# Kernel tuning notes

Hardware: AMD Instinct MI355X
Metric: run time of the kernel (lower is better)

Reference implementation:

```python
import jax, jax.numpy as jnp
import numpy as np

BT, N = 4, 2048
FIN, FOUT = 512, 128          # GGE in/out; FOUT == PPI output (GAGA constraint)
PIN, POUT = 256, 128          # PPIGE in/out
HEAD = 4
K = POUT // HEAD              # per-head dim = 32
NEG_SLOPE = 0.2
MASK_VAL = -1e30


def setup_inputs() -> dict:
    key = jax.random.key(0)
    ks = jax.random.split(key, 24)
    s = 0.05
    inp = {}
    inp["a"] = jax.random.normal(ks[0], (BT, FIN), jnp.float32)
    inp["bio_a"] = jax.random.normal(ks[1], (BT, N, PIN), jnp.float32)
    inp["A"] = jax.random.randint(ks[2], (BT, N, N), 0, 2, jnp.int32)
    inp["b"] = jax.random.normal(ks[3], (BT, FIN), jnp.float32)
    inp["bio_b"] = jax.random.normal(ks[4], (BT, N, PIN), jnp.float32)
    inp["B"] = jax.random.randint(ks[5], (BT, N, N), 0, 2, jnp.int32)
    # PPIGE_GAT params (shared across both graph branches)
    inp["initW"] = jax.random.normal(ks[6], (POUT, PIN), jnp.float32) * s
    inp["initb"] = jnp.zeros((POUT,), jnp.float32)
    inp["projW"] = jax.random.normal(ks[7], (POUT, POUT), jnp.float32) * s  # no bias
    inp["attw"] = jax.random.normal(ks[8], (HEAD, 2 * K), jnp.float32) * s  # per-head [2k]->1
    inp["attb"] = jnp.zeros((HEAD,), jnp.float32)
    # GGE params
    inp["ggeW1"] = jax.random.normal(ks[9], (128, FIN), jnp.float32) * s
    inp["ggeb1"] = jnp.zeros((128,), jnp.float32)
    inp["ggeW2"] = jax.random.normal(ks[10], (FOUT, 128), jnp.float32) * s
    inp["ggeb2"] = jnp.zeros((FOUT,), jnp.float32)
    # LED params (hidden = FOUT)
    inp["convW"] = jax.random.normal(ks[11], (2 * FOUT, 2 * FOUT), jnp.float32) * s  # k=1 conv
    inp["convb"] = jnp.zeros((2 * FOUT,), jnp.float32)
    inp["ledW1"] = jax.random.normal(ks[12], (FOUT, 4 * FOUT), jnp.float32) * s
    inp["ledb1"] = jnp.zeros((FOUT,), jnp.float32)
    inp["ledW2"] = jax.random.normal(ks[13], (2, FOUT), jnp.float32) * s
    inp["ledb2"] = jnp.zeros((2,), jnp.float32)
    return inp


def _gat_layer(x, adj_mask, projW, attw, attb):
    # x: [B,N,POUT]; adj_mask: [B,N,N] bool
    Bt, n, _ = x.shape
    xh = (x @ projW.T).reshape(Bt, n, HEAD, K).transpose(0, 2, 1, 3)  # [B,h,N,k]
    # score(i,j) = leaky_relu(w1.x_i + w2.x_j + b)  (equivalent to Linear on concat)
    s1 = jnp.einsum('bhnk,hk->bhn', xh, attw[:, :K])
    s2 = jnp.einsum('bhnk,hk->bhn', xh, attw[:, K:])
    scores = jax.nn.leaky_relu(
        s1[..., :, None] + s2[..., None, :] + attb[None, :, None, None], NEG_SLOPE)
    scores = jnp.where(adj_mask[:, None], scores, MASK_VAL)
    att = jax.nn.softmax(scores, axis=-1)                     # [B,h,N,N]
    out = jax.nn.relu(att @ xh)                               # [B,h,N,k]
    return out.transpose(0, 2, 1, 3).reshape(Bt, n, HEAD * K)


def _ppige(bio, adj, initW, initb, projW, attw, attb):
    x = bio @ initW.T + initb
    return _gat_layer(x, adj > 0, projW, attw, attb) + x      # residual; dropout=eval


def _gge(a, W1, b1, W2, b2):
    h = jax.nn.relu(a @ W1.T + b1)
    return jax.nn.relu(h @ W2.T + b2)


def _gaga(G, h):
    # G: [B,N,D], h: [B,D]
    att = jax.nn.softmax(jnp.einsum('bnd,bd->bn', G, h), axis=-1)
    return jnp.einsum('bnd,bn->bd', G, att)


def _led(ea, eb, convW, convb, W1, b1, W2, b2):
    # pointwise conv over the length-2 stack [ea, eb], then maxpool over length
    cnn = jnp.maximum(ea @ convW.T + convb, eb @ convW.T + convb)  # [B,2D]
    x = jax.nn.relu(jnp.concatenate([cnn, ea - eb], axis=1) @ W1.T + b1)
    return x @ W2.T + b2


def reference(a, bio_a, A, b, bio_b, B,
              initW, initb, projW, attw, attb,
              ggeW1, ggeb1, ggeW2, ggeb2,
              convW, convb, ledW1, ledb1, ledW2, ledb2):
    G_a = _ppige(bio_a, A, initW, initb, projW, attw, attb)
    G_b = _ppige(bio_b, B, initW, initb, projW, attw, attb)
    h_a = _gge(a, ggeW1, ggeb1, ggeW2, ggeb2)
    h_b = _gge(b, ggeW1, ggeb1, ggeW2, ggeb2)
    e_a = jnp.concatenate([h_a, _gaga(G_a, h_a)], axis=-1)
    e_b = jnp.concatenate([h_b, _gaga(G_b, h_b)], axis=-1)
    logits = _led(e_a, e_b, convW, convb, ledW1, ledb1, ledW2, ledb2)
    return jax.nn.log_softmax(logits, axis=-1)
```

## Files before the change

kernel.cpp:

```cpp
#include <hip/hip_runtime.h>
#include <hip/hip_bf16.h>
#include <math.h>

#define NN 2048
#define NEG 0.2f
#define LOG2E 1.44269504f

typedef short bf16x8 __attribute__((ext_vector_type(8)));
typedef float f32x16 __attribute__((ext_vector_type(16)));

__device__ __forceinline__ float dot4(float4 a, float4 b) {
  return a.x * b.x + a.y * b.y + a.z * b.z + a.w * b.w;
}

__device__ __forceinline__ unsigned short bfbits(float f) {
  union { __hip_bfloat16 b; unsigned short u; } c;
  c.b = __float2bfloat16(f);
  return c.u;
}

__global__ __launch_bounds__(256) void k12_fused(const float* __restrict__ bioA,
                                                 const float* __restrict__ bioB,
                                                 const float* __restrict__ initW,
                                                 const float* __restrict__ initb,
                                                 const float* __restrict__ projW,
                                                 const float* __restrict__ attw,
                                                 const float* __restrict__ a_in,
                                                 const float* __restrict__ b_in,
                                                 const float* __restrict__ ggeW1,
                                                 const float* __restrict__ ggeb1,
                                                 const float* __restrict__ ggeW2,
                                                 const float* __restrict__ ggeb2,
                                                 float* __restrict__ xout,
                                                 unsigned short* __restrict__ xhT2,
                                                 float* __restrict__ s1,
                                                 float* __restrict__ s2,
                                                 float* __restrict__ hvbuf,
                                                 float* __restrict__ e) {
  __shared__ float As[32][36];
  __shared__ float Ws[32][132];
  __shared__ float xT[128][36];
  const int t = threadIdx.x;
  const int wave = t >> 6, lane = t & 63;

  if (blockIdx.x >= 512) {
    float* inL = (float*)As;
    float* h1L = ((float*)As) + 512;
    const int bb2 = (int)blockIdx.x - 512;
    const int g = bb2 >> 2, b = bb2 & 3;
    const int gb2 = g * 4 + b;
    const float* inp = (g ? b_in : a_in) + b * 512;
    if (t < 128) *(float4*)&inL[t * 4] = *(const float4*)&inp[t * 4];
    __syncthreads();
    for (int p = 0; p < 16; ++p) {
      const int o0 = p * 8 + wave * 2;
      const float* w0 = &ggeW1[o0 * 512 + lane * 8];
      const float* w1 = &ggeW1[(o0 + 1) * 512 + lane * 8];
      const float4 i0v = *(const float4*)&inL[lane * 8];
      const float4 i1v = *(const float4*)&inL[lane * 8 + 4];
      float s0 = dot4(*(const float4*)&w0[0], i0v) + dot4(*(const float4*)&w0[4], i1v);
      float s1v = dot4(*(const float4*)&w1[0], i0v) + dot4(*(const float4*)&w1[4], i1v);
#pragma unroll
      for (int s = 1; s < 64; s <<= 1) { s0 += __shfl_xor(s0, s); s1v += __shfl_xor(s1v, s); }
      if (lane == 0) {
        h1L[o0] = fmaxf(s0 + ggeb1[o0], 0.f);
        h1L[o0 + 1] = fmaxf(s1v + ggeb1[o0 + 1], 0.f);
      }
    }
    __syncthreads();
    for (int p = 0; p < 16; ++p) {
      const int o0 = p * 8 + wave * 2;
      const float2 w0 = *(const float2*)&ggeW2[o0 * 128 + lane * 2];
      const float2 w1 = *(const float2*)&ggeW2[(o0 + 1) * 128 + lane * 2];
      const float2 hvv = *(const float2*)&h1L[lane * 2];
      float s0 = w0.x * hvv.x + w0.y * hvv.y;
      float s1v = w1.x * hvv.x + w1.y * hvv.y;
#pragma unroll
      for (int s = 1; s < 64; s <<= 1) { s0 += __shfl_xor(s0, s); s1v += __shfl_xor(s1v, s); }
      if (lane == 0) {
        const float v0 = fmaxf(s0 + ggeb2[o0], 0.f);
        const float v1 = fmaxf(s1v + ggeb2[o0 + 1], 0.f);
        hvbuf[gb2 * 128 + o0] = v0;
        hvbuf[gb2 * 128 + o0 + 1] = v1;
        e[gb2 * 256 + o0] = v0;
        e[gb2 * 256 + o0 + 1] = v1;
      }
    }
    return;
  }

  const int m0 = blockIdx.x * 32;
  const float* A = (m0 < 8192) ? bioA : bioB;
  const int arow0 = (m0 < 8192) ? m0 : (m0 - 8192);
  const int og = t & 31, ig = t >> 5;

  float acc[4][4] = {};
  for (int kt = 0; kt < 256; kt += 32) {
    __syncthreads();
    {
      const int r = t >> 3, kq = t & 7;
      const float4 v = *(const float4*)&A[(arow0 + r) * 256 + kt + kq * 4];
      As[kq * 4 + 0][r] = v.x; As[kq * 4 + 1][r] = v.y;
      As[kq * 4 + 2][r] = v.z; As[kq * 4 + 3][r] = v.w;
    }
#pragma unroll
    for (int u = 0; u < 4; ++u) {
      const int f = u * 256 + t;
      const int o = f >> 3, kq = f & 7;
      const float4 v = *(const float4*)&initW[o * 256 + kt + kq * 4];
      Ws[kq * 4 + 0][o] = v.x; Ws[kq * 4 + 1][o] = v.y;
      Ws[kq * 4 + 2][o] = v.z; Ws[kq * 4 + 3][o] = v.w;
    }
    __syncthreads();
#pragma unroll
    for (int kk = 0; kk < 32; ++kk) {
      const float4 a4 = *(const float4*)&As[kk][ig * 4];
      const float4 w4 = *(const float4*)&Ws[kk][og * 4];
      const float av[4] = {a4.x, a4.y, a4.z, a4.w};
      const float wv[4] = {w4.x, w4.y, w4.z, w4.w};
#pragma unroll
      for (int ii = 0; ii < 4; ++ii)
#pragma unroll
        for (int jj = 0; jj < 4; ++jj) acc[ii][jj] += av[ii] * wv[jj];
    }
  }
  {
    const float4 b4 = *(const float4*)&initb[og * 4];
    const float bj[4] = {b4.x, b4.y, b4.z, b4.w};
#pragma unroll
    for (int ii = 0; ii < 4; ++ii) {
      const int row = m0 + ig * 4 + ii;
      float4 o4;
      o4.x = acc[ii][0] + bj[0]; o4.y = acc[ii][1] + bj[1];
      o4.z = acc[ii][2] + bj[2]; o4.w = acc[ii][3] + bj[3];
      *(float4*)&xout[row * 128 + og * 4] = o4;
    }
#pragma unroll
    for (int jj = 0; jj < 4; ++jj) {
      float4 v;
      v.x = acc[0][jj] + bj[jj]; v.y = acc[1][jj] + bj[jj];
      v.z = acc[2][jj] + bj[jj]; v.w = acc[3][jj] + bj[jj];
      *(float4*)&xT[og * 4 + jj][ig * 4] = v;
    }
  }
  __syncthreads();

  float acc2[4][4] = {};
  for (int kt = 0; kt < 128; kt += 32) {
    __syncthreads();
#pragma unroll
    for (int u = 0; u < 4; ++u) {
      const int f = u * 256 + t;
      const int o = f >> 3, kq = f & 7;
      const float4 v = *(const float4*)&projW[o * 128 + kt + kq * 4];
      Ws[kq * 4 + 0][o] = v.x; Ws[kq * 4 + 1][o] = v.y;
      Ws[kq * 4 + 2][o] = v.z; Ws[kq * 4 + 3][o] = v.w;
    }
    __syncthreads();
#pragma unroll
    for (int kk = 0; kk < 32; ++kk) {
      const float4 a4 = *(const float4*)&xT[kt + kk][ig * 4];
      const float4 w4 = *(const float4*)&Ws[kk][og * 4];
      const float av[4] = {a4.x, a4.y, a4.z, a4.w};
      const float wv[4] = {w4.x, w4.y, w4.z, w4.w};
#pragma unroll
      for (int ii = 0; ii < 4; ++ii)
#pragma unroll
        for (int jj = 0; jj < 4; ++jj) acc2[ii][jj] += av[ii] * wv[jj];
    }
  }
  const int h = og >> 3;
  const int k4i = (og & 7) * 4;
  const int g = m0 >> 13;
  const int bb = (m0 >> 11) & 3;
  const int gb = g * 4 + bb;
  const int n0 = (m0 & 2047) + ig * 4;
  const float4 w1 = *(const float4*)&attw[h * 64 + k4i];
  const float4 w2 = *(const float4*)&attw[h * 64 + 32 + k4i];
  float p1[4], p2[4];
#pragma unroll
  for (int ii = 0; ii < 4; ++ii) {
    float4 v;
    v.x = acc2[ii][0]; v.y = acc2[ii][1]; v.z = acc2[ii][2]; v.w = acc2[ii][3];
    p1[ii] = dot4(v, w1);
    p2[ii] = dot4(v, w2);
  }
  {
    const int mtile = n0 >> 4, jslot = (n0 >> 3) & 1, j8 = n0 & 7;
    const int base2 = ((((gb * 4 + h) * 128 + mtile) * 2 + jslot) * 32) * 8 + j8;
#pragma unroll
    for (int jj = 0; jj < 4; ++jj) {
      const int kin = k4i + jj;
      ushort4 u;
      u.x = bfbits(acc2[0][jj]); u.y = bfbits(acc2[1][jj]);
      u.z = bfbits(acc2[2][jj]); u.w = bfbits(acc2[3][jj]);
      *(ushort4*)&xhT2[base2 + kin * 8] = u;
    }
  }
#pragma unroll
  for (int s = 1; s < 8; s <<= 1) {
#pragma unroll
    for (int ii = 0; ii < 4; ++ii) {
      p1[ii] += __shfl_xor(p1[ii], s);
      p2[ii] += __shfl_xor(p2[ii], s);
    }
  }
  if ((og & 7) == 0) {
#pragma unroll
    for (int ii = 0; ii < 4; ++ii) {
      s1[(gb * 4 + h) * NN + n0 + ii] = p1[ii];
      s2[(gb * 4 + h) * NN + n0 + ii] = p2[ii];
    }
  }
}

#define K3_PROLOGUE                                                           \
  {                                                                           \
    const float* s2g = s2w + gb * 4 * NN;                                     \
    _Pragma("unroll")                                                         \
    for (int u = 0; u < 4; ++u) {                                             \
      const int idx = u * 2048 + t * 4;                                       \
      float4 v = *(const float4*)&s2g[idx];                                   \
      v.x *= LOG2E; v.y *= LOG2E; v.z *= LOG2E; v.w *= LOG2E;                 \
      *(float4*)&s2L[idx] = v;                                                \
    }                                                                         \
  }                                                                           \
  _Pragma("unroll")                                                           \
  for (int r4 = 0; r4 < 4; ++r4) {                                            \
    const int r = wave * 4 + r4;                                              \
    const int* arow = adj + r * NN;                                           \
    int av[32];                                                               \
    _Pragma("unroll")                                                         \
    for (int w = 0; w < 32; ++w) av[w] = __builtin_nontemporal_load(&arow[w * 64 + lane]); \
    _Pragma("unroll")                                                         \
    for (int w = 0; w < 32; ++w) {                                            \
      const unsigned long long mm = __ballot(av[w] > 0);                      \
      if (lane < 2) adjL[r * 66 + 2 * w + lane] = (unsigned int)(mm >> (32 * lane)); \
    }                                                                         \
  }

#define K3_SCORE_BODY(MM)                                                     \
    const int j0 = jlo + 16 * (MM) + jslot * 8;                               \
    const unsigned int wbits = adjL[i * 66 + ((jlo + 16 * (MM)) >> 5)];       \
    const unsigned int bits8 = wbits >> ((((MM) & 1) * 16) + jslot * 8);      \
    const float4 s2a = *(const float4*)&s2L[h * 2048 + j0];                   \
    const float4 s2b = *(const float4*)&s2L[h * 2048 + j0 + 4];               \
    const float sv[8] = {s2a.x, s2a.y, s2a.z, s2a.w,                          \
                         s2b.x, s2b.y, s2b.z, s2b.w};                         \
    union { bf16x8 v; unsigned short u[8]; } af;                              \
    float dsum = 0.f;                                                         \
    _Pragma("unroll")                                                         \
    for (int e = 0; e < 8; ++e) {                                             \
      float s = sc1v + sv[e];                                                 \
      s = fmaxf(s, NEG * s);                                                  \
      float pe = __builtin_amdgcn_exp2f(s);                                   \
      pe = ((bits8 >> e) & 1u) ? pe : 0.f;                                    \
      af.u[e] = bfbits(pe);                                                   \
      dsum += pe;                                                             \
    }                                                                         \
    den += dsum;

__global__ __launch_bounds__(512) void k3_attn(const unsigned short* __restrict__ xhT2,
                                               const float* __restrict__ s1w,
                                               const float* __restrict__ s2w,
                                               const int* __restrict__ adjA,
                                               const int* __restrict__ adjB,
                                               const float* __restrict__ attb,
                                               const float* __restrict__ x,
                                               const float* __restrict__ hv,
                                               float* __restrict__ G,
                                               float* __restrict__ wsumC,
                                               float* __restrict__ mzC) {
  __shared__ __align__(16) unsigned char smem3[42240];
  unsigned int* adjL = (unsigned int*)smem3;
  float* s2L = (float*)(smem3 + 8448);
  float* denR = (float*)(smem3 + 41216);
  float* accR = (float*)smem3;
  float* lgW = (float*)(smem3 + 16640);
  float* pL = (float*)(smem3 + 17280);

  const int t = threadIdx.x;
  const int wave = t >> 6, lane = t & 63;
  const int p = (int)blockIdx.x;
  const int blk = (p & 7) * 64 + (p >> 3);
  const int g = blk >> 8, b = (blk >> 6) & 3;
  const int i0 = (blk & 63) * 32;
  const int gb = g * 4 + b;
  const int cidx = gb * 64 + (blk & 63);
  const int* adj = (g ? adjB : adjA) + (b * NN + i0) * NN;
  K3_PROLOGUE
  __syncthreads();

  const int h = wave & 3;
  const int jhalf = wave >> 2;
  const int jlo = jhalf * 1024;
  const int i = lane & 31;
  const int jslot = lane >> 5;
  const float sc1v = (s1w[(gb * 4 + h) * NN + i0 + i] + attb[h]) * LOG2E;
  const unsigned short* bbase = xhT2 + (gb * 4 + h) * 65536 + jhalf * 32768 + lane * 8;
  f32x16 acc = {0.f, 0.f, 0.f, 0.f, 0.f, 0.f, 0.f, 0.f,
                0.f, 0.f, 0.f, 0.f, 0.f, 0.f, 0.f, 0.f};
  float den = 0.f;

#define K3_CSTEP(RB, MM)                                                      \
  {                                                                           \
    K3_SCORE_BODY(MM)                                                         \
    acc = __builtin_amdgcn_mfma_f32_32x32x16_bf16(af.v, RB, acc, 0, 0, 0);    \
  }

  bf16x8 fa0 = *(const bf16x8*)&bbase[0 * 512];
  bf16x8 fa1 = *(const bf16x8*)&bbase[1 * 512];
  bf16x8 fa2 = *(const bf16x8*)&bbase[2 * 512];
  bf16x8 fa3 = *(const bf16x8*)&bbase[3 * 512];
  bf16x8 fb0 = *(const bf16x8*)&bbase[4 * 512];
  bf16x8 fb1 = *(const bf16x8*)&bbase[5 * 512];
  bf16x8 fb2 = *(const bf16x8*)&bbase[6 * 512];
  bf16x8 fb3 = *(const bf16x8*)&bbase[7 * 512];
  bf16x8 fc0 = *(const bf16x8*)&bbase[8 * 512];
  bf16x8 fc1 = *(const bf16x8*)&bbase[9 * 512];
  bf16x8 fc2 = *(const bf16x8*)&bbase[10 * 512];
  bf16x8 fc3 = *(const bf16x8*)&bbase[11 * 512];
  bf16x8 fd0 = *(const bf16x8*)&bbase[12 * 512];
  bf16x8 fd1 = *(const bf16x8*)&bbase[13 * 512];
  bf16x8 fd2 = *(const bf16x8*)&bbase[14 * 512];
  bf16x8 fd3 = *(const bf16x8*)&bbase[15 * 512];
  __builtin_amdgcn_sched_barrier(0);
  for (int mb = 0; mb < 64; mb += 16) {
    K3_CSTEP(fa0, mb + 0)
    K3_CSTEP(fa1, mb + 1)
    K3_CSTEP(fa2, mb + 2)
    K3_CSTEP(fa3, mb + 3)
    __builtin_amdgcn_sched_barrier(0);
    if (mb < 48) {
      fa0 = *(const bf16x8*)&bbase[(mb + 16) * 512];
      fa1 = *(const bf16x8*)&bbase[(mb + 17) * 512];
      fa2 = *(const bf16x8*)&bbase[(mb + 18) * 512];
      fa3 = *(const bf16x8*)&bbase[(mb + 19) * 512];
    }
    __builtin_amdgcn_sched_barrier(0);
    K3_CSTEP(fb0, mb + 4)
    K3_CSTEP(fb1, mb + 5)
    K3_CSTEP(fb2, mb + 6)
    K3_CSTEP(fb3, mb + 7)
    __builtin_amdgcn_sched_barrier(0);
    if (mb < 48) {
      fb0 = *(const bf16x8*)&bbase[(mb + 20) * 512];
      fb1 = *(const bf16x8*)&bbase[(mb + 21) * 512];
      fb2 = *(const bf16x8*)&bbase[(mb + 22) * 512];
      fb3 = *(const bf16x8*)&bbase[(mb + 23) * 512];
    }
    __builtin_amdgcn_sched_barrier(0);
    K3_CSTEP(fc0, mb + 8)
    K3_CSTEP(fc1, mb + 9)
    K3_CSTEP(fc2, mb + 10)
    K3_CSTEP(fc3, mb + 11)
    __builtin_amdgcn_sched_barrier(0);
    if (mb < 48) {
      fc0 = *(const bf16x8*)&bbase[(mb + 24) * 512];
      fc1 = *(const bf16x8*)&bbase[(mb + 25) * 512];
      fc2 = *(const bf16x8*)&bbase[(mb + 26) * 512];
      fc3 = *(const bf16x8*)&bbase[(mb + 27) * 512];
    }
    __builtin_amdgcn_sched_barrier(0);
    K3_CSTEP(fd0, mb + 12)
    K3_CSTEP(fd1, mb + 13)
    K3_CSTEP(fd2, mb + 14)
    K3_CSTEP(fd3, mb + 15)
    __builtin_amdgcn_sched_barrier(0);
    if (mb < 48) {
      fd0 = *(const bf16x8*)&bbase[(mb + 28) * 512];
      fd1 = *(const bf16x8*)&bbase[(mb + 29) * 512];
      fd2 = *(const bf16x8*)&bbase[(mb + 30) * 512];
      fd3 = *(const bf16x8*)&bbase[(mb + 31) * 512];
    }
    __builtin_amdgcn_sched_barrier(0);
  }
#undef K3_CSTEP

  den += __shfl_xor(den, 32);
  if (lane < 32) denR[(h * 2 + jhalf) * 32 + lane] = den;
  __syncthreads();
  if (jhalf == 1) {
#pragma unroll
    for (int r = 0; r < 16; ++r) accR[(h * 16 + r) * 65 + lane] = acc[r];
  }
  __syncthreads();
  const float hvv = hv[gb * 128 + h * 32 + i];
  if (jhalf == 0) {
#pragma unroll
    for (int r = 0; r < 16; ++r) {
      const int row = (r & 3) + 8 * (r >> 2) + 4 * jslot;
      const float dinv = 1.f / (denR[(h * 2 + 0) * 32 + row] + denR[(h * 2 + 1) * 32 + row]);
      const int off = (gb * NN + i0 + row) * 128 + h * 32 + i;
      const float av2 = acc[r] + accR[(h * 16 + r) * 65 + lane];
      const float gval = fmaxf(av2 * dinv, 0.f) + x[off];
      G[off] = gval;
      float c = gval * hvv;
      c += __shfl_xor(c, 1); c += __shfl_xor(c, 2); c += __shfl_xor(c, 4);
      c += __shfl_xor(c, 8); c += __shfl_xor(c, 16);
      if (i == 0) lgW[h * 32 + row] = c;
    }
  }
  __syncthreads();
  if (t < 32) {
    float lg = lgW[t] + lgW[32 + t] + lgW[64 + t] + lgW[96 + t];
    float m = lg;
    m = fmaxf(m, __shfl_xor(m, 1)); m = fmaxf(m, __shfl_xor(m, 2));
    m = fmaxf(m, __shfl_xor(m, 4)); m = fmaxf(m, __shfl_xor(m, 8));
    m = fmaxf(m, __shfl_xor(m, 16));
    const float pv = __expf(lg - m);
    float z = pv;
    z += __shfl_xor(z, 1); z += __shfl_xor(z, 2); z += __shfl_xor(z, 4);
    z += __shfl_xor(z, 8); z += __shfl_xor(z, 16);
    pL[t] = pv;
    if (t == 0) { mzC[cidx * 2] = m; mzC[cidx * 2 + 1] = z; }
  }
  __syncthreads();
  if (jhalf == 0) {
    float wp = 0.f;
#pragma unroll
    for (int r = 0; r < 16; ++r) {
      const int row = (r & 3) + 8 * (r >> 2) + 4 * jslot;
      const int off = (gb * NN + i0 + row) * 128 + h * 32 + i;
      wp += pL[row] * G[off];
    }
    wp += __shfl_xor(wp, 32);
    if (jslot == 0) wsumC[cidx * 128 + h * 32 + i] = wp;
  }
}

__global__ __launch_bounds__(256) void k5_led(const float* __restrict__ e,
                                              const float* __restrict__ wsumC,
                                              const float* __restrict__ mzC,
                                              const float* __restrict__ convW,
                                              const float* __restrict__ convb,
                                              const float* __restrict__ ledW1,
                                              const float* __restrict__ ledb1,
                                              const float* __restrict__ ledW2,
                                              const float* __restrict__ ledb2,
                                              float* __restrict__ out) {
  __shared__ float eaL[256], ebL[256], uL[512], xL[128], lgL[2];
  const int t = threadIdx.x;
  const int wave = t >> 6, lane = t & 63;
  const int bt = blockIdx.x;
  const int gba = bt, gbb = 4 + bt;
  if (t < 128) {
    eaL[t] = e[gba * 256 + t];
    ebL[t] = e[gbb * 256 + t];
    float ma = -1e30f, mb2 = -1e30f;
    for (int c = 0; c < 64; ++c) {
      ma = fmaxf(ma, mzC[(gba * 64 + c) * 2]);
      mb2 = fmaxf(mb2, mzC[(gbb * 64 + c) * 2]);
    }
    float Za = 0.f, Zb = 0.f, sa = 0.f, sb = 0.f;
    for (int c = 0; c < 64; ++c) {
      const float wa = __expf(mzC[(gba * 64 + c) * 2] - ma);
      const float wb = __expf(mzC[(gbb * 64 + c) * 2] - mb2);
      Za += mzC[(gba * 64 + c) * 2 + 1] * wa;
      Zb += mzC[(gbb * 64 + c) * 2 + 1] * wb;
      sa += wsumC[(gba * 64 + c) * 128 + t] * wa;
      sb += wsumC[(gbb * 64 + c) * 128 + t] * wb;
    }
    eaL[128 + t] = sa / Za;
    ebL[128 + t] = sb / Zb;
  }
  __syncthreads();
  uL[256 + t] = eaL[t] - ebL[t];
  const float4 ea4 = *(const float4*)&eaL[lane * 4];
  const float4 eb4 = *(const float4*)&ebL[lane * 4];
  for (int p = 0; p < 32; ++p) {
    const int o0 = p * 8 + wave * 2;
    const float4 w0 = *(const float4*)&convW[o0 * 256 + lane * 4];
    const float4 w1 = *(const float4*)&convW[(o0 + 1) * 256 + lane * 4];
    float sa0 = dot4(w0, ea4), sb0 = dot4(w0, eb4);
    float sa1 = dot4(w1, ea4), sb1 = dot4(w1, eb4);
#pragma unroll
    for (int s = 1; s < 64; s <<= 1) {
      sa0 += __shfl_xor(sa0, s); sb0 += __shfl_xor(sb0, s);
      sa1 += __shfl_xor(sa1, s); sb1 += __shfl_xor(sb1, s);
    }
    if (lane == 0) {
      const float c0 = convb[o0], c1 = convb[o0 + 1];
      uL[o0] = fmaxf(sa0 + c0, sb0 + c0);
      uL[o0 + 1] = fmaxf(sa1 + c1, sb1 + c1);
    }
  }
  __syncthreads();
  for (int p = 0; p < 16; ++p) {
    const int o0 = p * 8 + wave * 2;
    const float* w0 = &ledW1[o0 * 512 + lane * 8];
    const float* w1 = &ledW1[(o0 + 1) * 512 + lane * 8];
    const float4 u0 = *(const float4*)&uL[lane * 8];
    const float4 u1 = *(const float4*)&uL[lane * 8 + 4];
    float s0 = dot4(*(const float4*)&w0[0], u0) + dot4(*(const float4*)&w0[4], u1);
    float s1v = dot4(*(const float4*)&w1[0], u0) + dot4(*(const float4*)&w1[4], u1);
#pragma unroll
    for (int s = 1; s < 64; s <<= 1) { s0 += __shfl_xor(s0, s); s1v += __shfl_xor(s1v, s); }
    if (lane == 0) {
      xL[o0] = fmaxf(s0 + ledb1[o0], 0.f);
      xL[o0 + 1] = fmaxf(s1v + ledb1[o0 + 1], 0.f);
    }
  }
  __syncthreads();
  if (wave < 2) {
    const float2 w = *(const float2*)&ledW2[wave * 128 + lane * 2];
    const float2 xv = *(const float2*)&xL[lane * 2];
    float s0 = w.x * xv.x + w.y * xv.y;
#pragma unroll
    for (int s = 1; s < 64; s <<= 1) s0 += __shfl_xor(s0, s);
    if (lane == 0) lgL[wave] = s0 + ledb2[wave];
  }
  __syncthreads();
  if (t == 0) {
    const float l0 = lgL[0], l1 = lgL[1];
    const float m = fmaxf(l0, l1);
    const float za = __expf(l0 - m) + __expf(l1 - m);
    const float lz = __logf(za);
    out[bt * 2 + 0] = l0 - m - lz;
    out[bt * 2 + 1] = l1 - m - lz;
  }
}

extern "C" void kernel_launch(void* const* d_in, const int* in_sizes, int n_in,
                              void* d_out, int out_size, void* d_ws, size_t ws_size,
                              hipStream_t stream) {
  (void)in_sizes; (void)n_in; (void)out_size; (void)ws_size;
  const float* a     = (const float*)d_in[0];
  const float* bioA  = (const float*)d_in[1];
  const int*   A     = (const int*)d_in[2];
  const float* b     = (const float*)d_in[3];
  const float* bioB  = (const float*)d_in[4];
  const int*   B     = (const int*)d_in[5];
  const float* initW = (const float*)d_in[6];
  const float* initb = (const float*)d_in[7];
  const float* projW = (const float*)d_in[8];
  const float* attw  = (const float*)d_in[9];
  const float* attb  = (const float*)d_in[10];
  const float* ggeW1 = (const float*)d_in[11];
  const float* ggeb1 = (const float*)d_in[12];
  const float* ggeW2 = (const float*)d_in[13];
  const float* ggeb2 = (const float*)d_in[14];
  const float* convW = (const float*)d_in[15];
  const float* convb = (const float*)d_in[16];
  const float* ledW1 = (const float*)d_in[17];
  const float* ledb1 = (const float*)d_in[18];
  const float* ledW2 = (const float*)d_in[19];
  const float* ledb2 = (const float*)d_in[20];

  float* ws = (float*)d_ws;
  float*          x     = ws;
  unsigned short* xhT2  = (unsigned short*)(ws + 2097152);
  float*          s1    = ws + 3145728;
  float*          s2    = ws + 3211264;
  float*          G     = ws + 3276800;
  float*          mzC   = ws + 5373952;
  float*          wsumC = ws + 5374976;
  float*          hv    = ws + 5440512;
  float*          e     = ws + 5441536;
  float* out = (float*)d_out;

  k12_fused<<<520, 256, 0, stream>>>(bioA, bioB, initW, initb, projW, attw,
                                     a, b, ggeW1, ggeb1, ggeW2, ggeb2,
                                     x, xhT2, s1, s2, hv, e);
  k3_attn<<<512, 512, 0, stream>>>(xhT2, s1, s2, A, B, attb, x, hv, G,
                                   wsumC, mzC);
  k5_led<<<4, 256, 0, stream>>>(e, wsumC, mzC, convW, convb, ledW1, ledb1,
                                ledW2, ledb2, out);
}
```

Baseline: 165.0 us.

## Move adjacency bit-packing from attention kernel into projection kernel

```diff
diff --git a/kernel.cpp b/kernel.cpp
--- a/kernel.cpp
+++ b/kernel.cpp
@@ -31,6 +31,9 @@
                                                  const float* __restrict__ ggeb1,
                                                  const float* __restrict__ ggeW2,
                                                  const float* __restrict__ ggeb2,
+                                                 const int* __restrict__ adjA,
+                                                 const int* __restrict__ adjB,
+                                                 unsigned int* __restrict__ adjP,
                                                  float* __restrict__ xout,
                                                  unsigned short* __restrict__ xhT2,
                                                  float* __restrict__ s1,
@@ -42,18 +45,19 @@
   __shared__ float xT[128][36];
   const int t = threadIdx.x;
   const int wave = t >> 6, lane = t & 63;
-
-  if (blockIdx.x >= 512) {
+  const int p = (int)blockIdx.x;
+
+  if (p >= 1024) {
     float* inL = (float*)As;
     float* h1L = ((float*)As) + 512;
-    const int bb2 = (int)blockIdx.x - 512;
+    const int bb2 = p - 1024;
     const int g = bb2 >> 2, b = bb2 & 3;
     const int gb2 = g * 4 + b;
     const float* inp = (g ? b_in : a_in) + b * 512;
     if (t < 128) *(float4*)&inL[t * 4] = *(const float4*)&inp[t * 4];
     __syncthreads();
-    for (int p = 0; p < 16; ++p) {
-      const int o0 = p * 8 + wave * 2;
+    for (int q = 0; q < 16; ++q) {
+      const int o0 = q * 8 + wave * 2;
       const float* w0 = &ggeW1[o0 * 512 + lane * 8];
       const float* w1 = &ggeW1[(o0 + 1) * 512 + lane * 8];
       const float4 i0v = *(const float4*)&inL[lane * 8];
@@ -68,8 +72,8 @@
       }
     }
     __syncthreads();
-    for (int p = 0; p < 16; ++p) {
-      const int o0 = p * 8 + wave * 2;
+    for (int q = 0; q < 16; ++q) {
+      const int o0 = q * 8 + wave * 2;
       const float2 w0 = *(const float2*)&ggeW2[o0 * 128 + lane * 2];
       const float2 w1 = *(const float2*)&ggeW2[(o0 + 1) * 128 + lane * 2];
       const float2 hvv = *(const float2*)&h1L[lane * 2];
@@ -89,7 +93,30 @@
     return;
   }
 
-  const int m0 = blockIdx.x * 32;
+  if (p & 1) {
+    const int pb = p >> 1;
+    const int g = pb >> 8, b = (pb >> 6) & 3;
+    const int i0 = (pb & 63) * 32;
+    const int* adj = (g ? adjB : adjA) + (b * NN + i0) * NN;
+    unsigned int* dst = adjP + pb * 2048;
+#pragma unroll
+    for (int r8 = 0; r8 < 8; ++r8) {
+      const int r = wave * 8 + r8;
+      const int* arow = adj + r * NN;
+      int av[32];
+#pragma unroll
+      for (int w = 0; w < 32; ++w)
+        av[w] = __builtin_nontemporal_load(&arow[w * 64 + lane]);
+#pragma unroll
+      for (int w = 0; w < 32; ++w) {
+        const unsigned long long mm = __ballot(av[w] > 0);
+        if (lane < 2) dst[r * 64 + 2 * w + lane] = (unsigned int)(mm >> (32 * lane));
+      }
+    }
+    return;
+  }
+
+  const int m0 = (p >> 1) * 32;
   const float* A = (m0 < 8192) ? bioA : bioB;
   const int arow0 = (m0 < 8192) ? m0 : (m0 - 8192);
   const int og = t & 31, ig = t >> 5;
@@ -213,31 +240,6 @@
     }
   }
 }
-
-#define K3_PROLOGUE                                                           \
-  {                                                                           \
-    const float* s2g = s2w + gb * 4 * NN;                                     \
-    _Pragma("unroll")                                                         \
-    for (int u = 0; u < 4; ++u) {                                             \
-      const int idx = u * 2048 + t * 4;                                       \
-      float4 v = *(const float4*)&s2g[idx];                                   \
-      v.x *= LOG2E; v.y *= LOG2E; v.z *= LOG2E; v.w *= LOG2E;                 \
-      *(float4*)&s2L[idx] = v;                                                \
-    }                                                                         \
-  }                                                                           \
-  _Pragma("unroll")                                                           \
-  for (int r4 = 0; r4 < 4; ++r4) {                                            \
-    const int r = wave * 4 + r4;                                              \
-    const int* arow = adj + r * NN;                                           \
-    int av[32];                                                               \
-    _Pragma("unroll")                                                         \
-    for (int w = 0; w < 32; ++w) av[w] = __builtin_nontemporal_load(&arow[w * 64 + lane]); \
-    _Pragma("unroll")                                                         \
-    for (int w = 0; w < 32; ++w) {                                            \
-      const unsigned long long mm = __ballot(av[w] > 0);                      \
-      if (lane < 2) adjL[r * 66 + 2 * w + lane] = (unsigned int)(mm >> (32 * lane)); \
-    }                                                                         \
-  }
 
 #define K3_SCORE_BODY(MM)                                                     \
     const int j0 = jlo + 16 * (MM) + jslot * 8;                               \
@@ -263,8 +265,7 @@
 __global__ __launch_bounds__(512) void k3_attn(const unsigned short* __restrict__ xhT2,
                                                const float* __restrict__ s1w,
                                                const float* __restrict__ s2w,
-                                               const int* __restrict__ adjA,
-                                               const int* __restrict__ adjB,
+                                               const unsigned int* __restrict__ adjP,
                                                const float* __restrict__ attb,
                                                const float* __restrict__ x,
                                                const float* __restrict__ hv,
@@ -287,8 +288,23 @@
   const int i0 = (blk & 63) * 32;
   const int gb = g * 4 + b;
   const int cidx = gb * 64 + (blk & 63);
-  const int* adj = (g ? adjB : adjA) + (b * NN + i0) * NN;
-  K3_PROLOGUE
+  {
+    const float* s2g = s2w + gb * 4 * NN;
+#pragma unroll
+    for (int u = 0; u < 4; ++u) {
+      const int idx = u * 2048 + t * 4;
+      float4 v = *(const float4*)&s2g[idx];
+      v.x *= LOG2E; v.y *= LOG2E; v.z *= LOG2E; v.w *= LOG2E;
+      *(float4*)&s2L[idx] = v;
+    }
+    const int q0 = t * 4;
+    const int4 v = *(const int4*)&adjP[cidx * 2048 + q0];
+    const int rr = q0 >> 6, ww = q0 & 63;
+    adjL[rr * 66 + ww + 0] = (unsigned int)v.x;
+    adjL[rr * 66 + ww + 1] = (unsigned int)v.y;
+    adjL[rr * 66 + ww + 2] = (unsigned int)v.z;
+    adjL[rr * 66 + ww + 3] = (unsigned int)v.w;
+  }
   __syncthreads();
 
   const int h = wave & 3;
@@ -557,12 +573,14 @@
   float*          wsumC = ws + 5374976;
   float*          hv    = ws + 5440512;
   float*          e     = ws + 5441536;
+  unsigned int*   adjP  = (unsigned int*)(ws + 5443584);
   float* out = (float*)d_out;
 
-  k12_fused<<<520, 256, 0, stream>>>(bioA, bioB, initW, initb, projW, attw,
-                                     a, b, ggeW1, ggeb1, ggeW2, ggeb2,
-                                     x, xhT2, s1, s2, hv, e);
-  k3_attn<<<512, 512, 0, stream>>>(xhT2, s1, s2, A, B, attb, x, hv, G,
+  k12_fused<<<1032, 256, 0, stream>>>(bioA, bioB, initW, initb, projW, attw,
+                                      a, b, ggeW1, ggeb1, ggeW2, ggeb2,
+                                      A, B, adjP,
+                                      x, xhT2, s1, s2, hv, e);
+  k3_attn<<<512, 512, 0, stream>>>(xhT2, s1, s2, adjP, attb, x, hv, G,
                                    wsumC, mzC);
   k5_led<<<4, 256, 0, stream>>>(e, wsumC, mzC, convW, convb, ledW1, ledb1,
                                 ledW2, ledb2, out);
```

Result: slower. 168.4 us (+2.0%).
